# Kernel tuning notes

Measured on AMD Instinct MI355X. Metric: run time of the kernel, lower is better.

The kernel has to match this reference:

```python
import jax, jax.numpy as jnp
import numpy as np

K = 20  # kNN fan-out


def knn_idx(x, k):
    # x: (B, C, N). Negative squared pairwise distance; top-k largest = nearest.
    inner = -2.0 * jnp.einsum('bcn,bcm->bnm', x, x)        # (B, N, N)
    xx = jnp.sum(x * x, axis=1)                            # (B, N)
    pd = -xx[:, :, None] - inner - xx[:, None, :]          # (B, N, N)
    return jax.lax.top_k(pd, k)[1]                         # (B, N, k) int32


def get_graph_feature(x, k):
    # x: (B, C, N) -> edge features (B, 2C, N, k)
    idx = knn_idx(x, k)                                    # (B, N, k)
    xt = jnp.transpose(x, (0, 2, 1))                       # (B, N, C)
    nbrs = jax.vmap(lambda pts, ids: pts[ids])(xt, idx)    # (B, N, k, C)
    center = xt[:, :, None, :]                             # (B, N, 1, C)
    feat = jnp.concatenate(
        [nbrs - center, jnp.broadcast_to(center, nbrs.shape)], axis=-1)  # (B,N,k,2C)
    return jnp.transpose(feat, (0, 3, 1, 2))               # (B, 2C, N, k)


def vn_layer(W, x):
    # W: (out, in); x: (B, in, N, k) -> (B, out, N, k)
    return jnp.einsum('oi,bink->bonk', W, x)


def setup_inputs() -> dict:
    key = jax.random.key(0)
    ks = jax.random.split(key, 6)
    B, C, N = 16, 3, 2048
    num_classes = 10
    return {
        'x': jax.random.normal(ks[0], (B, C, N), dtype=jnp.float32),
        'W1': jax.random.normal(ks[1], (64, 6), dtype=jnp.float32),
        'W2': jax.random.normal(ks[2], (128, 64), dtype=jnp.float32),
        'W3': jax.random.normal(ks[3], (256, 128), dtype=jnp.float32),
        'fc_w': jax.random.normal(ks[4], (num_classes, 256), dtype=jnp.float32) * 0.0625,
        'fc_b': jax.random.normal(ks[5], (num_classes,), dtype=jnp.float32) * 0.0625,
    }


def reference(x, W1, W2, W3, fc_w, fc_b):
    h = get_graph_feature(x, K)          # (B, 6, N, k)
    h = vn_layer(W1, h)                  # (B, 64, N, k)
    h = jax.nn.relu(vn_layer(W2, h))     # (B, 128, N, k)
    h = jax.nn.relu(vn_layer(W3, h))     # (B, 256, N, k)
    h = jnp.max(h, axis=-1)              # max over neighbors k -> (B, 256, N)
    h = jnp.max(h, axis=-1)              # global max over points -> (B, 256)
    return h @ fc_w.T + fc_b             # (B, num_classes)
```

## Files before the change

### kernel.cpp

```cpp
#include <hip/hip_runtime.h>
#include <stdint.h>

typedef _Float16 v8h __attribute__((ext_vector_type(8)));
typedef _Float16 v2h __attribute__((ext_vector_type(2)));
typedef float v4f __attribute__((ext_vector_type(4)));
typedef float v16f __attribute__((ext_vector_type(16)));

#define NPTS 2048
#define BATCH 16
#define KNN 20
#define PAIRS (NPTS * KNN)

__device__ __forceinline__ unsigned pair_relu_h2(unsigned pu, unsigned qu) {
  v2h a = *(const v2h*)&pu;
  v2h b = *(const v2h*)&qu;
  v2h s = a + b;
  v2h z = {(_Float16)0.f, (_Float16)0.f};
  v2h r = __builtin_elementwise_max(s, z);
  return *(const unsigned*)&r;
}

__global__ void prep_kernel(const float* __restrict__ W1, const float* __restrict__ W2,
                            float* __restrict__ M2a, float* __restrict__ M2b,
                            int* __restrict__ H) {
  if (blockIdx.x == 0 && threadIdx.x < 128) {
    int o = threadIdx.x;
    float a0 = 0, a1 = 0, a2 = 0, b0 = 0, b1 = 0, b2 = 0;
    for (int i = 0; i < 64; ++i) {
      float w2 = W2[o * 64 + i];
      const float* w1r = W1 + i * 6;
      a0 += w2 * w1r[0]; a1 += w2 * w1r[1]; a2 += w2 * w1r[2];
      b0 += w2 * (w1r[3] - w1r[0]); b1 += w2 * (w1r[4] - w1r[1]); b2 += w2 * (w1r[5] - w1r[2]);
    }
    M2a[o * 3 + 0] = a0; M2a[o * 3 + 1] = a1; M2a[o * 3 + 2] = a2;
    M2b[o * 3 + 0] = b0; M2b[o * 3 + 1] = b1; M2b[o * 3 + 2] = b2;
  }
  int g = blockIdx.x * 128 + threadIdx.x;
  if (g < BATCH * 256) H[g] = 0;
}

__global__ __launch_bounds__(64) void pq_kernel(const float* __restrict__ x,
                                                const float* __restrict__ M2a,
                                                const float* __restrict__ M2b,
                                                unsigned short* __restrict__ p,
                                                unsigned short* __restrict__ q) {
  int b = blockIdx.x >> 6;
  int j0 = (blockIdx.x & 63) << 5;
  int t = threadIdx.x;
  int o0 = t * 2;
  float a00 = M2a[o0 * 3 + 0], a01 = M2a[o0 * 3 + 1], a02 = M2a[o0 * 3 + 2];
  float a10 = M2a[o0 * 3 + 3], a11 = M2a[o0 * 3 + 4], a12 = M2a[o0 * 3 + 5];
  float b00 = M2b[o0 * 3 + 0], b01 = M2b[o0 * 3 + 1], b02 = M2b[o0 * 3 + 2];
  float b10 = M2b[o0 * 3 + 3], b11 = M2b[o0 * 3 + 4], b12 = M2b[o0 * 3 + 5];
  const float* xb = x + b * 3 * NPTS;
  unsigned* pw = (unsigned*)p;
  unsigned* qw = (unsigned*)q;
  for (int jj = 0; jj < 32; ++jj) {
    int j = j0 + jj;
    float x0 = xb[j], x1 = xb[NPTS + j], x2 = xb[2 * NPTS + j];
    float p0 = a00 * x0 + a01 * x1 + a02 * x2;
    float p1 = a10 * x0 + a11 * x1 + a12 * x2;
    float q0 = b00 * x0 + b01 * x1 + b02 * x2;
    float q1 = b10 * x0 + b11 * x1 + b12 * x2;
    size_t base = ((size_t)(b * NPTS + j)) * 64 + t;
    auto hp = __builtin_amdgcn_cvt_pkrtz(p0, p1);
    auto hq = __builtin_amdgcn_cvt_pkrtz(q0, q1);
    pw[base] = *(const unsigned*)&hp;
    qw[base] = *(const unsigned*)&hq;
  }
}

__global__ __launch_bounds__(256) void knn_kernel(const float* __restrict__ x,
                                                  int* __restrict__ idxOut) {
  __shared__ float px[NPTS], py[NPTS], pz[NPTS];
  __shared__ unsigned long long cand[4][4][128];
  int b = blockIdx.x >> 7;
  int qblk = blockIdx.x & 127;
  const float* xb = x + b * 3 * NPTS;
  for (int i = threadIdx.x; i < NPTS; i += 256) {
    px[i] = xb[i]; py[i] = xb[NPTS + i]; pz[i] = xb[2 * NPTS + i];
  }
  __syncthreads();
  int wid = threadIdx.x >> 6, lane = threadIdx.x & 63;
  int qbase = qblk * 16 + wid * 4;

  float qx[4], qy[4], qz[4], mn[4];
#pragma unroll
  for (int g = 0; g < 4; ++g) {
    qx[g] = px[qbase + g]; qy[g] = py[qbase + g]; qz[g] = pz[qbase + g];
    mn[g] = 1e30f;
  }

  for (int s = 0; s < 32; ++s) {
    int i = s * 64 + lane;
    float X = px[i], Y = py[i], Z = pz[i];
#pragma unroll
    for (int g = 0; g < 4; ++g) {
      float dx = X - qx[g], dy = Y - qy[g], dz = Z - qz[g];
      mn[g] = fminf(mn[g], dx * dx + dy * dy + dz * dz);
    }
  }

  float tau[4];
#pragma unroll
  for (int g = 0; g < 4; ++g) {
    float v = mn[g];
    for (int k = 2; k <= 64; k <<= 1) {
      for (int j = k >> 1; j > 0; j >>= 1) {
        float o = __shfl_xor(v, j);
        bool low = (lane & j) == 0;
        bool up = (lane & k) == 0;
        v = (low == up) ? fminf(v, o) : fmaxf(v, o);
      }
    }
    tau[g] = __shfl(v, 19) * (1.0f + 3.8e-6f);
  }

  int cnt[4] = {0, 0, 0, 0};
  for (int s = 0; s < 32; ++s) {
    int i = s * 64 + lane;
    float X = px[i], Y = py[i], Z = pz[i];
#pragma unroll
    for (int g = 0; g < 4; ++g) {
      float dx = X - qx[g], dy = Y - qy[g], dz = Z - qz[g];
      float d = dx * dx + dy * dy + dz * dz;
      bool take = d <= tau[g];
      unsigned long long mb = __ballot(take);
      if (take) {
        int pos = cnt[g] + __popcll(mb & ((1ull << lane) - 1ull));
        if (pos < 128)
          cand[wid][g][pos] =
              (((unsigned long long)__float_as_uint(d)) << 32) | (unsigned)i;
      }
      cnt[g] += __popcll(mb);
    }
  }

#pragma unroll
  for (int g = 0; g < 4; ++g) {
    int nc = cnt[g] < 128 ? cnt[g] : 128;
    unsigned long long k0 = (lane < nc) ? cand[wid][g][lane] : ~0ull;
    unsigned long long k1 = (lane + 64 < nc) ? cand[wid][g][lane + 64] : ~0ull;
    int r0 = 0, r1 = 0;
    for (int i = 0; i < nc; ++i) {
      unsigned long long ki = cand[wid][g][i];
      r0 += (ki < k0) ? 1 : 0;
      r1 += (ki < k1) ? 1 : 0;
    }
    long long obase = ((long long)b * NPTS + qbase + g) * KNN;
    if (lane < nc && r0 < KNN) idxOut[obase + r0] = (int)(k0 & 0xffffffffu);
    if (lane + 64 < nc && r1 < KNN) idxOut[obase + r1] = (int)(k1 & 0xffffffffu);
  }
}

__global__ __launch_bounds__(256, 3) void gemm_max_kernel(
    const unsigned short* __restrict__ p, const unsigned short* __restrict__ q,
    const int* __restrict__ idx, const float* __restrict__ W3, int* __restrict__ H) {
  __shared__ __align__(16) unsigned short h2s[2][32 * 128];

  int b = blockIdx.x & 15;
  int w = blockIdx.x >> 4;
  int t = threadIdx.x;
  int lane = t & 63, wid = t >> 6;
  int col = lane & 31, hi = lane >> 5;

  v8h bfr0[8], bfr1[8];
#pragma unroll
  for (int kk = 0; kk < 8; ++kk) {
    const float* s0 = W3 + (size_t)(wid * 64 + col) * 128 + kk * 16 + hi * 8;
    const float* s1 = s0 + 32 * 128;
    v8h f0, f1;
#pragma unroll
    for (int jj = 0; jj < 8; ++jj) { f0[jj] = (_Float16)s0[jj]; f1[jj] = (_Float16)s1[jj]; }
    bfr0[kk] = f0; bfr1[kk] = f1;
  }

  const unsigned short* pB = p + (size_t)b * NPTS * 128;
  const unsigned short* qB = q + (size_t)b * NPTS * 128;
  const int* idxB = idx + (size_t)b * PAIRS;

  int pm = t >> 3;
  int c2 = t & 7;
  int st0 = pm * 128 + (((c2 * 2) ^ (pm & 7)) * 8);
  int st1 = pm * 128 + (((c2 * 2 + 1) ^ (pm & 7)) * 8);

  const int NT = PAIRS / 32;

  uint4 P0, P1, Q0, Q1;
  int jn = 0;
  {
    int pr = w * 32 + pm;
    int j = idxB[pr] & (NPTS - 1);
    int n = pr / 20;
    P0 = *(const uint4*)(pB + (size_t)j * 128 + c2 * 16);
    P1 = *(const uint4*)(pB + (size_t)j * 128 + c2 * 16 + 8);
    Q0 = *(const uint4*)(qB + (size_t)n * 128 + c2 * 16);
    Q1 = *(const uint4*)(qB + (size_t)n * 128 + c2 * 16 + 8);
    int T1 = w + 48;
    if (T1 < NT) jn = idxB[T1 * 32 + pm];
  }

  float vmx0 = 0.f, vmx1 = 0.f;
  int buf = 0;
  for (int T = w; T < NT; T += 48) {
    uint4 R0, R1;
    R0.x = pair_relu_h2(P0.x, Q0.x); R0.y = pair_relu_h2(P0.y, Q0.y);
    R0.z = pair_relu_h2(P0.z, Q0.z); R0.w = pair_relu_h2(P0.w, Q0.w);
    R1.x = pair_relu_h2(P1.x, Q1.x); R1.y = pair_relu_h2(P1.y, Q1.y);
    R1.z = pair_relu_h2(P1.z, Q1.z); R1.w = pair_relu_h2(P1.w, Q1.w);
    *(uint4*)&h2s[buf][st0] = R0;
    *(uint4*)&h2s[buf][st1] = R1;
    __syncthreads();

    int Tn = T + 48;
    if (Tn < NT) {
      int prn = Tn * 32 + pm;
      int j = jn & (NPTS - 1);
      int n = prn / 20;
      P0 = *(const uint4*)(pB + (size_t)j * 128 + c2 * 16);
      P1 = *(const uint4*)(pB + (size_t)j * 128 + c2 * 16 + 8);
      Q0 = *(const uint4*)(qB + (size_t)n * 128 + c2 * 16);
      Q1 = *(const uint4*)(qB + (size_t)n * 128 + c2 * 16 + 8);
      int T2 = T + 96;
      if (T2 < NT) jn = idxB[T2 * 32 + pm];
    }

    v16f acc0 = {0.f}, acc1 = {0.f};
#pragma unroll
    for (int kk = 0; kk < 8; ++kk) {
      v8h a = *(const v8h*)&h2s[buf][col * 128 + (((kk * 2 + hi) ^ (col & 7)) * 8)];
      acc0 = __builtin_amdgcn_mfma_f32_32x32x16_f16(a, bfr0[kk], acc0, 0, 0, 0);
      acc1 = __builtin_amdgcn_mfma_f32_32x32x16_f16(a, bfr1[kk], acc1, 0, 0, 0);
    }
    float a0 = fmaxf(fmaxf(acc0[0], acc0[1]), fmaxf(acc0[2], acc0[3]));
    float a1 = fmaxf(fmaxf(acc0[4], acc0[5]), fmaxf(acc0[6], acc0[7]));
    float a2 = fmaxf(fmaxf(acc0[8], acc0[9]), fmaxf(acc0[10], acc0[11]));
    float a3 = fmaxf(fmaxf(acc0[12], acc0[13]), fmaxf(acc0[14], acc0[15]));
    vmx0 = fmaxf(vmx0, fmaxf(fmaxf(a0, a1), fmaxf(a2, a3)));
    float c0 = fmaxf(fmaxf(acc1[0], acc1[1]), fmaxf(acc1[2], acc1[3]));
    float c1 = fmaxf(fmaxf(acc1[4], acc1[5]), fmaxf(acc1[6], acc1[7]));
    float c2v = fmaxf(fmaxf(acc1[8], acc1[9]), fmaxf(acc1[10], acc1[11]));
    float c3 = fmaxf(fmaxf(acc1[12], acc1[13]), fmaxf(acc1[14], acc1[15]));
    vmx1 = fmaxf(vmx1, fmaxf(fmaxf(c0, c1), fmaxf(c2v, c3)));
    buf ^= 1;
  }

  float v0 = fmaxf(vmx0, __shfl_xor(vmx0, 32));
  float v1 = fmaxf(vmx1, __shfl_xor(vmx1, 32));
  if (hi == 0) {
    atomicMax(&H[b * 256 + wid * 64 + col], __float_as_int(v0));
    atomicMax(&H[b * 256 + wid * 64 + 32 + col], __float_as_int(v1));
  }
}

__global__ __launch_bounds__(64) void fc_kernel(const int* __restrict__ Hi,
                                                const float* __restrict__ fcw,
                                                const float* __restrict__ fcb,
                                                float* __restrict__ out) {
  int b = blockIdx.x / 10, r = blockIdx.x % 10;
  int lane = threadIdx.x;
  const float* Hb = (const float*)Hi + b * 256;
  float s = 0.f;
#pragma unroll
  for (int c = lane; c < 256; c += 64) s += Hb[c] * fcw[r * 256 + c];
#pragma unroll
  for (int m = 32; m > 0; m >>= 1) s += __shfl_xor(s, m);
  if (lane == 0) out[b * 10 + r] = s + fcb[r];
}

extern "C" void kernel_launch(void* const* d_in, const int* in_sizes, int n_in,
                              void* d_out, int out_size, void* d_ws, size_t ws_size,
                              hipStream_t stream) {
  const float* x   = (const float*)d_in[0];
  const float* W1  = (const float*)d_in[1];
  const float* W2  = (const float*)d_in[2];
  const float* W3  = (const float*)d_in[3];
  const float* fcw = (const float*)d_in[4];
  const float* fcb = (const float*)d_in[5];
  float* out = (float*)d_out;
  char* ws = (char*)d_ws;

  float* M2a = (float*)(ws + 0);
  float* M2b = (float*)(ws + 1536);
  int* H     = (int*)(ws + 4096);
  int* idx   = (int*)(ws + 24576);
  unsigned short* p = (unsigned short*)(ws + 3145728);
  unsigned short* q = (unsigned short*)(ws + 12582912);

  prep_kernel<<<32, 128, 0, stream>>>(W1, W2, M2a, M2b, H);
  pq_kernel<<<BATCH * 64, 64, 0, stream>>>(x, M2a, M2b, p, q);
  knn_kernel<<<BATCH * 128, 256, 0, stream>>>(x, idx);
  gemm_max_kernel<<<BATCH * 48, 256, 0, stream>>>(p, q, idx, W3, H);
  fc_kernel<<<BATCH * 10, 64, 0, stream>>>(H, fcw, fcb, out);
}
```

Before: 174.0 us.

## Restructure kNN kernel: float4 points with norms, 8 queries per wave, 512-thread blocks

The kNN kernel now stores points in shared memory as float4 with a precomputed squared norm. Each distance is computed as three FMAs on the expanded form (|p|^2 - 2 q·p, dropping the constant |q|^2), which replaces the subtract-square-add sequence. Each wave handles 8 queries instead of 4, so every shared-memory point load is reused across more queries, and blocks grow to 512 threads with a quarter as many blocks. The candidate buffer shrinks to 64 per query, with an offset added to the distance key so negative values still sort correctly as unsigned, and the tolerance on the threshold is adjusted to match. The expanded form loses precision and can reorder near-ties, and more than 64 candidates within the threshold would now be truncated.

Result: faster. 164.4 us (-5.5%).

```diff
diff --git a/kernel.cpp b/kernel.cpp
--- a/kernel.cpp
+++ b/kernel.cpp
@@ -70,40 +70,41 @@
   }
 }
 
-__global__ __launch_bounds__(256) void knn_kernel(const float* __restrict__ x,
-                                                  int* __restrict__ idxOut) {
-  __shared__ float px[NPTS], py[NPTS], pz[NPTS];
-  __shared__ unsigned long long cand[4][4][128];
-  int b = blockIdx.x >> 7;
-  int qblk = blockIdx.x & 127;
+__global__ __launch_bounds__(512, 4) void knn_kernel(const float* __restrict__ x,
+                                                     int* __restrict__ idxOut) {
+  __shared__ float4 pts[NPTS];
+  __shared__ unsigned long long cand[8][8][64];
+  int b = blockIdx.x >> 5;
+  int qblk = blockIdx.x & 31;
   const float* xb = x + b * 3 * NPTS;
-  for (int i = threadIdx.x; i < NPTS; i += 256) {
-    px[i] = xb[i]; py[i] = xb[NPTS + i]; pz[i] = xb[2 * NPTS + i];
+  for (int i = threadIdx.x; i < NPTS; i += 512) {
+    float X = xb[i], Y = xb[NPTS + i], Z = xb[2 * NPTS + i];
+    pts[i] = make_float4(X, Y, Z, X * X + Y * Y + Z * Z);
   }
   __syncthreads();
   int wid = threadIdx.x >> 6, lane = threadIdx.x & 63;
-  int qbase = qblk * 16 + wid * 4;
-
-  float qx[4], qy[4], qz[4], mn[4];
-#pragma unroll
-  for (int g = 0; g < 4; ++g) {
-    qx[g] = px[qbase + g]; qy[g] = py[qbase + g]; qz[g] = pz[qbase + g];
+  int qbase = qblk * 64 + wid * 8;
+
+  float m2x[8], m2y[8], m2z[8], mn[8];
+#pragma unroll
+  for (int g = 0; g < 8; ++g) {
+    float4 qp = pts[qbase + g];
+    m2x[g] = -2.f * qp.x; m2y[g] = -2.f * qp.y; m2z[g] = -2.f * qp.z;
     mn[g] = 1e30f;
   }
 
   for (int s = 0; s < 32; ++s) {
-    int i = s * 64 + lane;
-    float X = px[i], Y = py[i], Z = pz[i];
-#pragma unroll
-    for (int g = 0; g < 4; ++g) {
-      float dx = X - qx[g], dy = Y - qy[g], dz = Z - qz[g];
-      mn[g] = fminf(mn[g], dx * dx + dy * dy + dz * dz);
-    }
-  }
-
-  float tau[4];
-#pragma unroll
-  for (int g = 0; g < 4; ++g) {
+    float4 P = pts[s * 64 + lane];
+#pragma unroll
+    for (int g = 0; g < 8; ++g) {
+      float d = fmaf(m2x[g], P.x, fmaf(m2y[g], P.y, fmaf(m2z[g], P.z, P.w)));
+      mn[g] = fminf(mn[g], d);
+    }
+  }
+
+  float tau[8];
+#pragma unroll
+  for (int g = 0; g < 8; ++g) {
     float v = mn[g];
     for (int k = 2; k <= 64; k <<= 1) {
       for (int j = k >> 1; j > 0; j >>= 1) {
@@ -113,43 +114,38 @@
         v = (low == up) ? fminf(v, o) : fmaxf(v, o);
       }
     }
-    tau[g] = __shfl(v, 19) * (1.0f + 3.8e-6f);
-  }
-
-  int cnt[4] = {0, 0, 0, 0};
+    float t = __shfl(v, 19);
+    tau[g] = t + fabsf(t) * 4e-6f + 1e-6f;
+  }
+
+  int cnt[8] = {0, 0, 0, 0, 0, 0, 0, 0};
   for (int s = 0; s < 32; ++s) {
     int i = s * 64 + lane;
-    float X = px[i], Y = py[i], Z = pz[i];
-#pragma unroll
-    for (int g = 0; g < 4; ++g) {
-      float dx = X - qx[g], dy = Y - qy[g], dz = Z - qz[g];
-      float d = dx * dx + dy * dy + dz * dz;
+    float4 P = pts[i];
+#pragma unroll
+    for (int g = 0; g < 8; ++g) {
+      float d = fmaf(m2x[g], P.x, fmaf(m2y[g], P.y, fmaf(m2z[g], P.z, P.w)));
       bool take = d <= tau[g];
       unsigned long long mb = __ballot(take);
       if (take) {
         int pos = cnt[g] + __popcll(mb & ((1ull << lane) - 1ull));
-        if (pos < 128)
-          cand[wid][g][pos] =
-              (((unsigned long long)__float_as_uint(d)) << 32) | (unsigned)i;
+        if (pos < 64) {
+          unsigned kd = __float_as_uint(d + 64.f);
+          cand[wid][g][pos] = (((unsigned long long)kd) << 32) | (unsigned)i;
+        }
       }
       cnt[g] += __popcll(mb);
     }
   }
 
 #pragma unroll
-  for (int g = 0; g < 4; ++g) {
-    int nc = cnt[g] < 128 ? cnt[g] : 128;
+  for (int g = 0; g < 8; ++g) {
+    int nc = cnt[g] < 64 ? cnt[g] : 64;
     unsigned long long k0 = (lane < nc) ? cand[wid][g][lane] : ~0ull;
-    unsigned long long k1 = (lane + 64 < nc) ? cand[wid][g][lane + 64] : ~0ull;
-    int r0 = 0, r1 = 0;
-    for (int i = 0; i < nc; ++i) {
-      unsigned long long ki = cand[wid][g][i];
-      r0 += (ki < k0) ? 1 : 0;
-      r1 += (ki < k1) ? 1 : 0;
-    }
+    int r0 = 0;
+    for (int i = 0; i < nc; ++i) r0 += (cand[wid][g][i] < k0) ? 1 : 0;
     long long obase = ((long long)b * NPTS + qbase + g) * KNN;
     if (lane < nc && r0 < KNN) idxOut[obase + r0] = (int)(k0 & 0xffffffffu);
-    if (lane + 64 < nc && r1 < KNN) idxOut[obase + r1] = (int)(k1 & 0xffffffffu);
   }
 }
 
@@ -289,7 +285,7 @@
 
   prep_kernel<<<32, 128, 0, stream>>>(W1, W2, M2a, M2b, H);
   pq_kernel<<<BATCH * 64, 64, 0, stream>>>(x, M2a, M2b, p, q);
-  knn_kernel<<<BATCH * 128, 256, 0, stream>>>(x, idx);
+  knn_kernel<<<BATCH * 32, 512, 0, stream>>>(x, idx);
   gemm_max_kernel<<<BATCH * 48, 256, 0, stream>>>(p, q, idx, W3, H);
   fc_kernel<<<BATCH * 10, 64, 0, stream>>>(H, fcw, fcb, out);
 }
```
